# Kernel optimization log

Hardware: AMD Instinct MI355X
Metric: run time of the kernel (lower is better)

The kernel has to match this reference:

```python
import jax, jax.numpy as jnp
import numpy as np

MIN_NORM = 1e-15
PROJ_EPS = 4e-3  # PoincareBall.proj eps for float32
C = 1.0          # curvature


def _artanh(x):
    return jnp.arctanh(jnp.clip(x, -1 + 1e-7, 1 - 1e-7))


def _mobius_add(x, y, c):
    x2 = jnp.sum(x * x, -1, keepdims=True)
    y2 = jnp.sum(y * y, -1, keepdims=True)
    xy = jnp.sum(x * y, -1, keepdims=True)
    num = (1 + 2 * c * xy + c * y2) * x + (1 - c * x2) * y
    denom = 1 + 2 * c * xy + c * c * x2 * y2
    return num / jnp.maximum(denom, MIN_NORM)


def _sqdist(p1, p2, c):
    sqrt_c = c ** 0.5
    ma = _mobius_add(-p1, p2, c)
    dist = _artanh(sqrt_c * jnp.linalg.norm(ma, axis=-1)) * 2.0 / sqrt_c
    return dist ** 2


def _logmap0(p, c):
    sqrt_c = c ** 0.5
    p_norm = jnp.maximum(jnp.linalg.norm(p, axis=-1, keepdims=True), MIN_NORM)
    return p / p_norm / sqrt_c * _artanh(sqrt_c * p_norm)


def _expmap0(u, c):
    sqrt_c = c ** 0.5
    u_norm = jnp.maximum(jnp.linalg.norm(u, axis=-1, keepdims=True), MIN_NORM)
    return jnp.tanh(sqrt_c * u_norm) * u / (sqrt_c * u_norm)


def _proj(x, c):
    norm = jnp.maximum(jnp.linalg.norm(x, axis=-1, keepdims=True), MIN_NORM)
    maxnorm = (1 - PROJ_EPS) / (c ** 0.5)
    return jnp.where(norm > maxnorm, x / norm * maxnorm, x)


def setup_inputs() -> dict:
    key = jax.random.key(0)
    k1, k2 = jax.random.split(key)
    N, D, E = 100000, 64, 1600000
    # points on the Poincare ball (small norms, then projected)
    x = _proj(0.01 * jax.random.normal(k1, (N, D), dtype=jnp.float32), C)
    edge_index = jax.random.randint(k2, (2, E), 0, N, dtype=jnp.int64)
    beta = jnp.full((1,), 1e-2, dtype=jnp.float32)  # HypAggAtt.beta param
    con = jnp.zeros((1,), dtype=jnp.float32)        # HypAggAtt.con param
    return {"x": x, "beta": beta, "con": con, "edge_index": edge_index}


def reference(x, beta, con, edge_index):
    c = C
    N = x.shape[0]
    row, col = edge_index[0], edge_index[1]
    # per-edge hyperbolic attention logits: exp(-beta * sqdist + con)
    dist = _sqdist(x[row], x[col], c)            # [E]
    edge_e = jnp.exp(-beta[0] * dist + con[0])   # [E]
    x_t = _logmap0(x, c)                         # [N, D] tangent features
    # SpecialSpmm: sparse(row,col,edge_e) @ x_t  -> scatter-add over rows
    support = jax.ops.segment_sum(edge_e[:, None] * x_t[col], row, num_segments=N)
    e_rowsum = jax.ops.segment_sum(edge_e, row, num_segments=N) + 1e-10
    support = support / e_rowsum[:, None]
    return _proj(_expmap0(support, c), c)
```

## Files before the change

kernel.cpp:

```cpp
#include <hip/hip_runtime.h>
#include <math.h>

#define D 64
#define MIN_NORM 1e-15f
#define PROJ_MAXNORM 0.996f
#define RPB 128
#define BINCAP 2560
#define MAXBIN 1024
#define EPB 4096
#define BT 512

typedef __attribute__((ext_vector_type(8))) short short8;
typedef __attribute__((ext_vector_type(4))) float float4_;

__device__ __forceinline__ float fast_artanh(float z) {
    z = fminf(z, 1.0f - 1e-7f);
    return 0.5f * __logf((1.0f + z) * __builtin_amdgcn_rcpf(1.0f - z));
}

__device__ __forceinline__ unsigned short f2bf(float x) {
    unsigned int b = __float_as_uint(x);
    return (unsigned short)((b + 0x7fffu + ((b >> 16) & 1u)) >> 16);
}

__device__ __forceinline__ float bf2f(unsigned short u) {
    return __uint_as_float(((unsigned int)u) << 16);
}

__global__ void bin_kernel(const float* __restrict__ x,
                           unsigned short* __restrict__ x_bf,
                           float2* __restrict__ snf,
                           const int* __restrict__ row_idx,
                           const int* __restrict__ col_idx,
                           int* __restrict__ cursor,
                           unsigned int* __restrict__ binData,
                           int E, int N, int nbins, int edgeBlocks) {
    __shared__ int hist[MAXBIN];
    __shared__ int base[MAXBIN];
    if ((int)blockIdx.x < edgeBlocks) {
        int e0 = blockIdx.x * EPB;
        int e1 = min(E, e0 + EPB);
        for (int i = threadIdx.x; i < nbins; i += BT) hist[i] = 0;
        __syncthreads();
        if (e1 - e0 == EPB) {
#pragma unroll
            for (int it = 0; it < EPB / (BT * 4); ++it) {
                int4 r = *(const int4*)(row_idx + e0 + it * (BT * 4) + (int)threadIdx.x * 4);
                atomicAdd(&hist[r.x >> 7], 1);
                atomicAdd(&hist[r.y >> 7], 1);
                atomicAdd(&hist[r.z >> 7], 1);
                atomicAdd(&hist[r.w >> 7], 1);
            }
        } else {
            for (int e = e0 + (int)threadIdx.x; e < e1; e += BT)
                atomicAdd(&hist[row_idx[e] >> 7], 1);
        }
        __syncthreads();
        for (int i = threadIdx.x; i < nbins; i += BT) {
            int h = hist[i];
            base[i] = h ? atomicAdd(&cursor[i], h) : 0;
        }
        __syncthreads();
        if (e1 - e0 == EPB) {
#pragma unroll
            for (int it = 0; it < EPB / (BT * 4); ++it) {
                int o = e0 + it * (BT * 4) + (int)threadIdx.x * 4;
                int4 r = *(const int4*)(row_idx + o);
                int4 c = *(const int4*)(col_idx + o);
                int b0 = r.x >> 7, b1 = r.y >> 7, b2 = r.z >> 7, b3 = r.w >> 7;
                int k0 = atomicAdd(&base[b0], 1);
                int k1 = atomicAdd(&base[b1], 1);
                int k2 = atomicAdd(&base[b2], 1);
                int k3 = atomicAdd(&base[b3], 1);
                if (k0 < BINCAP) binData[(size_t)b0 * BINCAP + k0] = ((unsigned int)(r.x & 127) << 17) | (unsigned int)c.x;
                if (k1 < BINCAP) binData[(size_t)b1 * BINCAP + k1] = ((unsigned int)(r.y & 127) << 17) | (unsigned int)c.y;
                if (k2 < BINCAP) binData[(size_t)b2 * BINCAP + k2] = ((unsigned int)(r.z & 127) << 17) | (unsigned int)c.z;
                if (k3 < BINCAP) binData[(size_t)b3 * BINCAP + k3] = ((unsigned int)(r.w & 127) << 17) | (unsigned int)c.w;
            }
        } else {
            for (int e = e0 + (int)threadIdx.x; e < e1; e += BT) {
                int r = row_idx[e];
                int c = col_idx[e];
                int b = r >> 7;
                int rk = atomicAdd(&base[b], 1);
                if (rk < BINCAP)
                    binData[(size_t)b * BINCAP + rk] =
                        ((unsigned int)(r & 127) << 17) | (unsigned int)c;
            }
        }
    } else {
        int nb = blockIdx.x - edgeBlocks;
        int node = nb * (BT / 16) + ((int)threadIdx.x >> 4);
        int j = threadIdx.x & 15;
        if (node >= N) return;
        float4 v = *((const float4*)(x + (size_t)node * D) + j);
        float s = v.x * v.x + v.y * v.y + v.z * v.z + v.w * v.w;
#pragma unroll
        for (int m = 1; m < 16; m <<= 1)
            s += __shfl_xor(s, m, 64);
        float pn = fmaxf(sqrtf(s), MIN_NORM);
        float f = fast_artanh(pn) / pn;
        ushort4 o;
        o.x = f2bf(v.x); o.y = f2bf(v.y); o.z = f2bf(v.z); o.w = f2bf(v.w);
        *((ushort4*)(x_bf + (size_t)node * D) + j) = o;
        if (j == 0) snf[node] = make_float2(s, f);
    }
}

__global__ void fused_kernel(const unsigned short* __restrict__ x_bf,
                             const float2* __restrict__ snf,
                             const unsigned int* __restrict__ binData,
                             const int* __restrict__ cursor,
                             const float* __restrict__ beta,
                             const float* __restrict__ con,
                             float* __restrict__ out, int N) {
    __shared__ int cnt[RPB];
    __shared__ int off[RPB];
    __shared__ int cur[RPB];
    __shared__ int tot[2];
    __shared__ int colsm[BINCAP];

    int b = blockIdx.x;
    int len = min(cursor[b], BINCAP);
    const unsigned int* bd = binData + (size_t)b * BINCAP;

    if (threadIdx.x < RPB) { cnt[threadIdx.x] = 0; cur[threadIdx.x] = 0; }
    if (threadIdx.x == 0) colsm[0] = 0;
    __syncthreads();
    for (int i = threadIdx.x; i < len; i += BT)
        atomicAdd(&cnt[bd[i] >> 17], 1);
    __syncthreads();
    if (threadIdx.x < RPB) {
        int v = cnt[threadIdx.x], inc = v;
#pragma unroll
        for (int m = 1; m < 64; m <<= 1) {
            int t = __shfl_up(inc, m, 64);
            if (((int)threadIdx.x & 63) >= m) inc += t;
        }
        off[threadIdx.x] = inc - v;
        if (((int)threadIdx.x & 63) == 63) tot[threadIdx.x >> 6] = inc;
    }
    __syncthreads();
    if (threadIdx.x >= 64 && threadIdx.x < RPB) off[threadIdx.x] += tot[0];
    __syncthreads();
    for (int i = threadIdx.x; i < len; i += BT) {
        unsigned int p = bd[i];
        int rl = p >> 17;
        int rk = atomicAdd(&cur[rl], 1);
        colsm[off[rl] + rk] = (int)(p & 0x1FFFFu);
    }
    __syncthreads();

    int wid = threadIdx.x >> 6;
    int lane = threadIdx.x & 63;
    int jj = lane & 15;
    int qd = lane >> 4;
    int src = ((jj >> 2) << 4) | jj;
    float Bc = beta[0], C0 = con[0];
    float4_ zero4 = {0.0f, 0.0f, 0.0f, 0.0f};

    int rl = wid * 16 + jj;
    int row = b * RPB + rl;
    int rlen = cnt[rl];
    int start = off[rl];
    int safe = rlen > 0 ? start + rlen - 1 : 0;

    int ml = rlen;
#pragma unroll
    for (int m = 1; m < 16; m <<= 1)
        ml = max(ml, __shfl_xor(ml, m, 64));

    const unsigned short* xr = x_bf + (size_t)row * D + qd * 8;
    short8 bfr0 = *(const short8*)xr;
    short8 bfr1 = *(const short8*)(xr + 32);
    float x2 = snf[row].x;

    float acc[16];
#pragma unroll
    for (int i = 0; i < 16; i++) acc[i] = 0.0f;
    float wacc = 0.0f;

    for (int t = 0; t < ml; ++t) {
        bool valid = t < rlen;
        int cw = colsm[valid ? start + t : safe];
        const unsigned short* rp = x_bf + (size_t)cw * D + qd * 8;
        short8 af0 = *(const short8*)rp;
        short8 af1 = *(const short8*)(rp + 32);
        float2 sf = snf[cw];

        float4_ d4 = __builtin_amdgcn_mfma_f32_16x16x32_bf16(af0, bfr0, zero4, 0, 0, 0);
        d4 = __builtin_amdgcn_mfma_f32_16x16x32_bf16(af1, bfr1, d4, 0, 0, 0);

        float sel01 = (jj & 1) ? d4[1] : d4[0];
        float sel23 = (jj & 1) ? d4[3] : d4[2];
        float dsel  = (jj & 2) ? sel23 : sel01;
        float d = __shfl(dsel, src, 64);

        float y2 = sf.x;
        float a_ = 1.0f - 2.0f * d + y2;
        float b_ = 1.0f - x2;
        float num2 = a_ * a_ * x2 - 2.0f * a_ * b_ * d + b_ * b_ * y2;
        float den = fmaxf(1.0f - 2.0f * d + x2 * y2, MIN_NORM);
        float man = sqrtf(fmaxf(num2, 0.0f)) * __builtin_amdgcn_rcpf(den);
        float at = fast_artanh(man);
        float w = __expf(-Bc * 4.0f * at * at + C0);
        w = valid ? w : 0.0f;
        float wf = w * sf.y;
        wacc += w;
#pragma unroll
        for (int j = 0; j < 8; j++) {
            acc[j]     += wf * bf2f((unsigned short)af0[j]);
            acc[8 + j] += wf * bf2f((unsigned short)af1[j]);
        }
    }

    float inv = __builtin_amdgcn_rcpf(wacc + 1e-10f);
    float s[16];
    float loc = 0.0f;
#pragma unroll
    for (int j = 0; j < 16; j++) {
        s[j] = acc[j] * inv;
        loc += s[j] * s[j];
    }
    loc += __shfl_xor(loc, 16, 64);
    loc += __shfl_xor(loc, 32, 64);
    float n2 = loc;
    float sq = sqrtf(n2);
    float un = fmaxf(sq, MIN_NORM);
    float e2 = __expf(2.0f * un);
    float th = (e2 - 1.0f) * __builtin_amdgcn_rcpf(e2 + 1.0f);
    float tt = th * __builtin_amdgcn_rcpf(un);
    float on = th * sq * __builtin_amdgcn_rcpf(un);
    float scale = tt;
    if (on > PROJ_MAXNORM)
        scale = tt / fmaxf(on, MIN_NORM) * PROJ_MAXNORM;

    if (row < N) {
        float* op = out + (size_t)row * D;
        float4 v0 = make_float4(scale * s[0],  scale * s[1],  scale * s[2],  scale * s[3]);
        float4 v1 = make_float4(scale * s[4],  scale * s[5],  scale * s[6],  scale * s[7]);
        float4 v2 = make_float4(scale * s[8],  scale * s[9],  scale * s[10], scale * s[11]);
        float4 v3 = make_float4(scale * s[12], scale * s[13], scale * s[14], scale * s[15]);
        *(float4*)(op + qd * 8)          = v0;
        *(float4*)(op + qd * 8 + 4)      = v1;
        *(float4*)(op + 32 + qd * 8)     = v2;
        *(float4*)(op + 32 + qd * 8 + 4) = v3;
    }
}

extern "C" void kernel_launch(void* const* d_in, const int* in_sizes, int n_in,
                              void* d_out, int out_size, void* d_ws, size_t ws_size,
                              hipStream_t stream) {
    const float* x    = (const float*)d_in[0];
    const float* beta = (const float*)d_in[1];
    const float* con  = (const float*)d_in[2];
    const int*   ei   = (const int*)d_in[3];

    int N = in_sizes[0] / D;
    int E = in_sizes[3] / 2;
    const int* row_idx = ei;
    const int* col_idx = ei + E;
    float* out = (float*)d_out;

    int nbins = (N + RPB - 1) / RPB;

    float2*         snf     = (float2*)d_ws;
    unsigned short* x_bf    = (unsigned short*)(snf + N);
    unsigned int*   binData = (unsigned int*)(x_bf + (size_t)N * D);
    int*            cursor  = (int*)(binData + (size_t)nbins * BINCAP);

    hipMemsetAsync(cursor, 0, (size_t)nbins * sizeof(int), stream);

    int edgeBlocks = (E + EPB - 1) / EPB;
    int nodeBlocks = (N + (BT / 16) - 1) / (BT / 16);

    bin_kernel<<<edgeBlocks + nodeBlocks, BT, 0, stream>>>(
        x, x_bf, snf, row_idx, col_idx, cursor, binData, E, N, nbins, edgeBlocks);

    fused_kernel<<<nbins, BT, 0, stream>>>(x_bf, snf, binData, cursor,
                                           beta, con, out, N);
}
```

Baseline: 176.3 us.

## Sort rows by degree per wave and software-pipeline neighbor gathers

Ranks the 128 rows in each bin by edge count and assigns them to waves in sorted order. Rows of similar length then share a 16-lane group, which cuts the idle iterations that come from looping to the group maximum. The inner edge loop now prefetches the next neighbor's bf16 features and norms while the current edge is computed, hiding gather latency. The cost is an O(RPB^2) ranking pass in shared memory, extra registers for the double-buffered operands, and one redundant prefetch at the end of each row.

```diff
diff --git a/kernel.cpp b/kernel.cpp
--- a/kernel.cpp
+++ b/kernel.cpp
@@ -118,6 +118,7 @@
     __shared__ int off[RPB];
     __shared__ int cur[RPB];
     __shared__ int tot[2];
+    __shared__ int srt[RPB];
     __shared__ int colsm[BINCAP];
 
     int b = blockIdx.x;
@@ -142,6 +143,15 @@
     }
     __syncthreads();
     if (threadIdx.x >= 64 && threadIdx.x < RPB) off[threadIdx.x] += tot[0];
+    if (threadIdx.x < RPB) {
+        unsigned int myKey = ((unsigned int)cnt[threadIdx.x] << 7) | (unsigned int)threadIdx.x;
+        int rank = 0;
+        for (int i = 0; i < RPB; ++i) {
+            unsigned int k = ((unsigned int)cnt[i] << 7) | (unsigned int)i;
+            rank += (k > myKey) ? 1 : 0;
+        }
+        srt[rank] = threadIdx.x;
+    }
     __syncthreads();
     for (int i = threadIdx.x; i < len; i += BT) {
         unsigned int p = bd[i];
@@ -159,7 +169,7 @@
     float Bc = beta[0], C0 = con[0];
     float4_ zero4 = {0.0f, 0.0f, 0.0f, 0.0f};
 
-    int rl = wid * 16 + jj;
+    int rl = srt[wid * 16 + jj];
     int row = b * RPB + rl;
     int rlen = cnt[rl];
     int start = off[rl];
@@ -180,37 +190,49 @@
     for (int i = 0; i < 16; i++) acc[i] = 0.0f;
     float wacc = 0.0f;
 
-    for (int t = 0; t < ml; ++t) {
-        bool valid = t < rlen;
-        int cw = colsm[valid ? start + t : safe];
+    if (ml > 0) {
+        int cw = colsm[rlen > 0 ? start : safe];
         const unsigned short* rp = x_bf + (size_t)cw * D + qd * 8;
-        short8 af0 = *(const short8*)rp;
-        short8 af1 = *(const short8*)(rp + 32);
-        float2 sf = snf[cw];
-
-        float4_ d4 = __builtin_amdgcn_mfma_f32_16x16x32_bf16(af0, bfr0, zero4, 0, 0, 0);
-        d4 = __builtin_amdgcn_mfma_f32_16x16x32_bf16(af1, bfr1, d4, 0, 0, 0);
-
-        float sel01 = (jj & 1) ? d4[1] : d4[0];
-        float sel23 = (jj & 1) ? d4[3] : d4[2];
-        float dsel  = (jj & 2) ? sel23 : sel01;
-        float d = __shfl(dsel, src, 64);
-
-        float y2 = sf.x;
-        float a_ = 1.0f - 2.0f * d + y2;
-        float b_ = 1.0f - x2;
-        float num2 = a_ * a_ * x2 - 2.0f * a_ * b_ * d + b_ * b_ * y2;
-        float den = fmaxf(1.0f - 2.0f * d + x2 * y2, MIN_NORM);
-        float man = sqrtf(fmaxf(num2, 0.0f)) * __builtin_amdgcn_rcpf(den);
-        float at = fast_artanh(man);
-        float w = __expf(-Bc * 4.0f * at * at + C0);
-        w = valid ? w : 0.0f;
-        float wf = w * sf.y;
-        wacc += w;
-#pragma unroll
-        for (int j = 0; j < 8; j++) {
-            acc[j]     += wf * bf2f((unsigned short)af0[j]);
-            acc[8 + j] += wf * bf2f((unsigned short)af1[j]);
+        short8 caf0 = *(const short8*)rp;
+        short8 caf1 = *(const short8*)(rp + 32);
+        float2 csf = snf[cw];
+
+        for (int t = 0; t < ml; ++t) {
+            int tn = t + 1;
+            int idxn = (tn < rlen) ? start + tn : safe;
+            int cwn = colsm[idxn];
+            const unsigned short* rpn = x_bf + (size_t)cwn * D + qd * 8;
+            short8 naf0 = *(const short8*)rpn;
+            short8 naf1 = *(const short8*)(rpn + 32);
+            float2 nsf = snf[cwn];
+
+            bool valid = t < rlen;
+            float4_ d4 = __builtin_amdgcn_mfma_f32_16x16x32_bf16(caf0, bfr0, zero4, 0, 0, 0);
+            d4 = __builtin_amdgcn_mfma_f32_16x16x32_bf16(caf1, bfr1, d4, 0, 0, 0);
+
+            float sel01 = (jj & 1) ? d4[1] : d4[0];
+            float sel23 = (jj & 1) ? d4[3] : d4[2];
+            float dsel  = (jj & 2) ? sel23 : sel01;
+            float d = __shfl(dsel, src, 64);
+
+            float y2 = csf.x;
+            float a_ = 1.0f - 2.0f * d + y2;
+            float b_ = 1.0f - x2;
+            float num2 = a_ * a_ * x2 - 2.0f * a_ * b_ * d + b_ * b_ * y2;
+            float den = fmaxf(1.0f - 2.0f * d + x2 * y2, MIN_NORM);
+            float man = sqrtf(fmaxf(num2, 0.0f)) * __builtin_amdgcn_rcpf(den);
+            float at = fast_artanh(man);
+            float w = __expf(-Bc * 4.0f * at * at + C0);
+            w = valid ? w : 0.0f;
+            float wf = w * csf.y;
+            wacc += w;
+#pragma unroll
+            for (int j = 0; j < 8; j++) {
+                acc[j]     += wf * bf2f((unsigned short)caf0[j]);
+                acc[8 + j] += wf * bf2f((unsigned short)caf1[j]);
+            }
+
+            caf0 = naf0; caf1 = naf1; csf = nsf;
         }
     }
 
```

After: 166.3 us. -5.7%, faster.

## Halve rows per bin, sort rows by degree, and prefetch neighbor gathers

Applied to the files above, without the earlier changes.

Bins now cover 64 rows instead of 128, and the fused kernel runs 256 threads, so there are twice as many smaller blocks. Within each block, rows are ranked by edge count so each 16-row MFMA group holds rows of similar degree, which cuts the padded iterations forced by the slowest row in the group. The edge loop is unrolled by two with software prefetch of the next neighbor's bf16 features and norms, to hide gather latency behind the compute. In exchange it adds an O(RPB) rank loop per thread, uses more registers, and the bin capacity becomes tighter at 1280 entries for 64 rows.

```diff
diff --git a/kernel.cpp b/kernel.cpp
--- a/kernel.cpp
+++ b/kernel.cpp
@@ -4,11 +4,12 @@
 #define D 64
 #define MIN_NORM 1e-15f
 #define PROJ_MAXNORM 0.996f
-#define RPB 128
-#define BINCAP 2560
-#define MAXBIN 1024
+#define RPB 64
+#define BINCAP 1280
+#define MAXBIN 2048
 #define EPB 4096
 #define BT 512
+#define FT 256
 
 typedef __attribute__((ext_vector_type(8))) short short8;
 typedef __attribute__((ext_vector_type(4))) float float4_;
@@ -46,14 +47,14 @@
 #pragma unroll
             for (int it = 0; it < EPB / (BT * 4); ++it) {
                 int4 r = *(const int4*)(row_idx + e0 + it * (BT * 4) + (int)threadIdx.x * 4);
-                atomicAdd(&hist[r.x >> 7], 1);
-                atomicAdd(&hist[r.y >> 7], 1);
-                atomicAdd(&hist[r.z >> 7], 1);
-                atomicAdd(&hist[r.w >> 7], 1);
+                atomicAdd(&hist[r.x >> 6], 1);
+                atomicAdd(&hist[r.y >> 6], 1);
+                atomicAdd(&hist[r.z >> 6], 1);
+                atomicAdd(&hist[r.w >> 6], 1);
             }
         } else {
             for (int e = e0 + (int)threadIdx.x; e < e1; e += BT)
-                atomicAdd(&hist[row_idx[e] >> 7], 1);
+                atomicAdd(&hist[row_idx[e] >> 6], 1);
         }
         __syncthreads();
         for (int i = threadIdx.x; i < nbins; i += BT) {
@@ -67,25 +68,25 @@
                 int o = e0 + it * (BT * 4) + (int)threadIdx.x * 4;
                 int4 r = *(const int4*)(row_idx + o);
                 int4 c = *(const int4*)(col_idx + o);
-                int b0 = r.x >> 7, b1 = r.y >> 7, b2 = r.z >> 7, b3 = r.w >> 7;
+                int b0 = r.x >> 6, b1 = r.y >> 6, b2 = r.z >> 6, b3 = r.w >> 6;
                 int k0 = atomicAdd(&base[b0], 1);
                 int k1 = atomicAdd(&base[b1], 1);
                 int k2 = atomicAdd(&base[b2], 1);
                 int k3 = atomicAdd(&base[b3], 1);
-                if (k0 < BINCAP) binData[(size_t)b0 * BINCAP + k0] = ((unsigned int)(r.x & 127) << 17) | (unsigned int)c.x;
-                if (k1 < BINCAP) binData[(size_t)b1 * BINCAP + k1] = ((unsigned int)(r.y & 127) << 17) | (unsigned int)c.y;
-                if (k2 < BINCAP) binData[(size_t)b2 * BINCAP + k2] = ((unsigned int)(r.z & 127) << 17) | (unsigned int)c.z;
-                if (k3 < BINCAP) binData[(size_t)b3 * BINCAP + k3] = ((unsigned int)(r.w & 127) << 17) | (unsigned int)c.w;
+                if (k0 < BINCAP) binData[(size_t)b0 * BINCAP + k0] = ((unsigned int)(r.x & 63) << 17) | (unsigned int)c.x;
+                if (k1 < BINCAP) binData[(size_t)b1 * BINCAP + k1] = ((unsigned int)(r.y & 63) << 17) | (unsigned int)c.y;
+                if (k2 < BINCAP) binData[(size_t)b2 * BINCAP + k2] = ((unsigned int)(r.z & 63) << 17) | (unsigned int)c.z;
+                if (k3 < BINCAP) binData[(size_t)b3 * BINCAP + k3] = ((unsigned int)(r.w & 63) << 17) | (unsigned int)c.w;
             }
         } else {
             for (int e = e0 + (int)threadIdx.x; e < e1; e += BT) {
                 int r = row_idx[e];
                 int c = col_idx[e];
-                int b = r >> 7;
+                int b = r >> 6;
                 int rk = atomicAdd(&base[b], 1);
                 if (rk < BINCAP)
                     binData[(size_t)b * BINCAP + rk] =
-                        ((unsigned int)(r & 127) << 17) | (unsigned int)c;
+                        ((unsigned int)(r & 63) << 17) | (unsigned int)c;
             }
         }
     } else {
@@ -106,6 +107,32 @@
         if (j == 0) snf[node] = make_float2(s, f);
     }
 }
+
+#define CHUNK_COMPUTE(AF0, AF1, SF, VALID)                                          \
+    {                                                                               \
+        float4_ d4 = __builtin_amdgcn_mfma_f32_16x16x32_bf16(AF0, bfr0, zero4, 0, 0, 0); \
+        d4 = __builtin_amdgcn_mfma_f32_16x16x32_bf16(AF1, bfr1, d4, 0, 0, 0);       \
+        float sel01 = (jj & 1) ? d4[1] : d4[0];                                     \
+        float sel23 = (jj & 1) ? d4[3] : d4[2];                                     \
+        float dsel  = (jj & 2) ? sel23 : sel01;                                     \
+        float d = __shfl(dsel, src, 64);                           \
+        float y2 = SF.x;                                                            \
+        float a_ = 1.0f - 2.0f * d + y2;                                            \
+        float b_ = 1.0f - x2;                                                       \
+        float num2 = a_ * a_ * x2 - 2.0f * a_ * b_ * d + b_ * b_ * y2;              \
+        float den = fmaxf(1.0f - 2.0f * d + x2 * y2, MIN_NORM);                     \
+        float man = sqrtf(fmaxf(num2, 0.0f)) * __builtin_amdgcn_rcpf(den);          \
+        float at = fast_artanh(man);                                                \
+        float w = __expf(-Bc * 4.0f * at * at + C0);                                \
+        w = (VALID) ? w : 0.0f;                                                     \
+        float wf = w * SF.y;                                                        \
+        wacc += w;                                                                  \
+        _Pragma("unroll")                                                           \
+        for (int j = 0; j < 8; j++) {                                               \
+            acc[j]     += wf * bf2f((unsigned short)AF0[j]);                        \
+            acc[8 + j] += wf * bf2f((unsigned short)AF1[j]);                        \
+        }                                                                           \
+    }
 
 __global__ void fused_kernel(const unsigned short* __restrict__ x_bf,
                              const float2* __restrict__ snf,
@@ -117,7 +144,7 @@
     __shared__ int cnt[RPB];
     __shared__ int off[RPB];
     __shared__ int cur[RPB];
-    __shared__ int tot[2];
+    __shared__ int srt[RPB];
     __shared__ int colsm[BINCAP];
 
     int b = blockIdx.x;
@@ -127,7 +154,7 @@
     if (threadIdx.x < RPB) { cnt[threadIdx.x] = 0; cur[threadIdx.x] = 0; }
     if (threadIdx.x == 0) colsm[0] = 0;
     __syncthreads();
-    for (int i = threadIdx.x; i < len; i += BT)
+    for (int i = threadIdx.x; i < len; i += FT)
         atomicAdd(&cnt[bd[i] >> 17], 1);
     __syncthreads();
     if (threadIdx.x < RPB) {
@@ -135,15 +162,19 @@
 #pragma unroll
         for (int m = 1; m < 64; m <<= 1) {
             int t = __shfl_up(inc, m, 64);
-            if (((int)threadIdx.x & 63) >= m) inc += t;
+            if ((int)threadIdx.x >= m) inc += t;
         }
         off[threadIdx.x] = inc - v;
-        if (((int)threadIdx.x & 63) == 63) tot[threadIdx.x >> 6] = inc;
+        unsigned int myKey = ((unsigned int)v << 6) | (unsigned int)threadIdx.x;
+        int rank = 0;
+        for (int i = 0; i < RPB; ++i) {
+            unsigned int k = ((unsigned int)cnt[i] << 6) | (unsigned int)i;
+            rank += (k > myKey) ? 1 : 0;
+        }
+        srt[rank] = threadIdx.x;
     }
     __syncthreads();
-    if (threadIdx.x >= 64 && threadIdx.x < RPB) off[threadIdx.x] += tot[0];
-    __syncthreads();
-    for (int i = threadIdx.x; i < len; i += BT) {
+    for (int i = threadIdx.x; i < len; i += FT) {
         unsigned int p = bd[i];
         int rl = p >> 17;
         int rk = atomicAdd(&cur[rl], 1);
@@ -159,7 +190,7 @@
     float Bc = beta[0], C0 = con[0];
     float4_ zero4 = {0.0f, 0.0f, 0.0f, 0.0f};
 
-    int rl = wid * 16 + jj;
+    int rl = srt[wid * 16 + jj];
     int row = b * RPB + rl;
     int rlen = cnt[rl];
     int start = off[rl];
@@ -180,47 +211,46 @@
     for (int i = 0; i < 16; i++) acc[i] = 0.0f;
     float wacc = 0.0f;
 
-    for (int t = 0; t < ml; ++t) {
-        bool valid = t < rlen;
-        int cw = colsm[valid ? start + t : safe];
-        const unsigned short* rp = x_bf + (size_t)cw * D + qd * 8;
-        short8 af0 = *(const short8*)rp;
-        short8 af1 = *(const short8*)(rp + 32);
-        float2 sf = snf[cw];
-
-        float4_ d4 = __builtin_amdgcn_mfma_f32_16x16x32_bf16(af0, bfr0, zero4, 0, 0, 0);
-        d4 = __builtin_amdgcn_mfma_f32_16x16x32_bf16(af1, bfr1, d4, 0, 0, 0);
-
-        float sel01 = (jj & 1) ? d4[1] : d4[0];
-        float sel23 = (jj & 1) ? d4[3] : d4[2];
-        float dsel  = (jj & 2) ? sel23 : sel01;
-        float d = __shfl(dsel, src, 64);
-
-        float y2 = sf.x;
-        float a_ = 1.0f - 2.0f * d + y2;
-        float b_ = 1.0f - x2;
-        float num2 = a_ * a_ * x2 - 2.0f * a_ * b_ * d + b_ * b_ * y2;
-        float den = fmaxf(1.0f - 2.0f * d + x2 * y2, MIN_NORM);
-        float man = sqrtf(fmaxf(num2, 0.0f)) * __builtin_amdgcn_rcpf(den);
-        float at = fast_artanh(man);
-        float w = __expf(-Bc * 4.0f * at * at + C0);
-        w = valid ? w : 0.0f;
-        float wf = w * sf.y;
-        wacc += w;
-#pragma unroll
-        for (int j = 0; j < 8; j++) {
-            acc[j]     += wf * bf2f((unsigned short)af0[j]);
-            acc[8 + j] += wf * bf2f((unsigned short)af1[j]);
+    if (ml > 0) {
+        int cwA = colsm[(0 < rlen) ? start : safe];
+        const unsigned short* rpA = x_bf + (size_t)cwA * D + qd * 8;
+        short8 afA0 = *(const short8*)rpA;
+        short8 afA1 = *(const short8*)(rpA + 32);
+        float2 sfA = snf[cwA];
+
+        int cwB = colsm[(1 < rlen) ? start + 1 : safe];
+        const unsigned short* rpB = x_bf + (size_t)cwB * D + qd * 8;
+        short8 afB0 = *(const short8*)rpB;
+        short8 afB1 = *(const short8*)(rpB + 32);
+        float2 sfB = snf[cwB];
+
+        for (int t = 0; t < ml; t += 2) {
+            int cw2 = colsm[(t + 2 < rlen) ? start + t + 2 : safe];
+            const unsigned short* rp2 = x_bf + (size_t)cw2 * D + qd * 8;
+            short8 nA0 = *(const short8*)rp2;
+            short8 nA1 = *(const short8*)(rp2 + 32);
+            float2 nsfA = snf[cw2];
+
+            CHUNK_COMPUTE(afA0, afA1, sfA, t < rlen);
+            afA0 = nA0; afA1 = nA1; sfA = nsfA;
+
+            int cw3 = colsm[(t + 3 < rlen) ? start + t + 3 : safe];
+            const unsigned short* rp3 = x_bf + (size_t)cw3 * D + qd * 8;
+            short8 nB0 = *(const short8*)rp3;
+            short8 nB1 = *(const short8*)(rp3 + 32);
+            float2 nsfB = snf[cw3];
+
+            CHUNK_COMPUTE(afB0, afB1, sfB, t + 1 < rlen);
+            afB0 = nB0; afB1 = nB1; sfB = nsfB;
         }
     }
 
     float inv = __builtin_amdgcn_rcpf(wacc + 1e-10f);
-    float s[16];
     float loc = 0.0f;
 #pragma unroll
     for (int j = 0; j < 16; j++) {
-        s[j] = acc[j] * inv;
-        loc += s[j] * s[j];
+        acc[j] *= inv;
+        loc += acc[j] * acc[j];
     }
     loc += __shfl_xor(loc, 16, 64);
     loc += __shfl_xor(loc, 32, 64);
@@ -237,10 +267,10 @@
 
     if (row < N) {
         float* op = out + (size_t)row * D;
-        float4 v0 = make_float4(scale * s[0],  scale * s[1],  scale * s[2],  scale * s[3]);
-        float4 v1 = make_float4(scale * s[4],  scale * s[5],  scale * s[6],  scale * s[7]);
-        float4 v2 = make_float4(scale * s[8],  scale * s[9],  scale * s[10], scale * s[11]);
-        float4 v3 = make_float4(scale * s[12], scale * s[13], scale * s[14], scale * s[15]);
+        float4 v0 = make_float4(scale * acc[0],  scale * acc[1],  scale * acc[2],  scale * acc[3]);
+        float4 v1 = make_float4(scale * acc[4],  scale * acc[5],  scale * acc[6],  scale * acc[7]);
+        float4 v2 = make_float4(scale * acc[8],  scale * acc[9],  scale * acc[10], scale * acc[11]);
+        float4 v3 = make_float4(scale * acc[12], scale * acc[13], scale * acc[14], scale * acc[15]);
         *(float4*)(op + qd * 8)          = v0;
         *(float4*)(op + qd * 8 + 4)      = v1;
         *(float4*)(op + 32 + qd * 8)     = v2;
@@ -277,6 +307,6 @@
     bin_kernel<<<edgeBlocks + nodeBlocks, BT, 0, stream>>>(
         x, x_bf, snf, row_idx, col_idx, cursor, binData, E, N, nbins, edgeBlocks);
 
-    fused_kernel<<<nbins, BT, 0, stream>>>(x_bf, snf, binData, cursor,
+    fused_kernel<<<nbins, FT, 0, stream>>>(x_bf, snf, binData, cursor,
                                            beta, con, out, N);
 }
```

Result: faster. 168.6 us (-4.4%).
